# Performance work log

Measured on AMD Instinct MI355X. Metric: run time of the kernel, lower is better.

Reference implementation:

```python
import jax, jax.numpy as jnp
import numpy as np

OUT_CAPS_NUM = 16
OUT_CAPS_DIM = 512
ITER_NUM = 3
EPS = 1e-7


def setup_inputs() -> dict:
    key = jax.random.key(0)
    k_x, k_w = jax.random.split(key)
    x = jax.random.normal(k_x, (32, 128, 1024), dtype=jnp.float32)
    # xavier_normal-ish scale so tanh is not saturated
    W = jax.random.normal(k_w, (1024, OUT_CAPS_NUM * OUT_CAPS_DIM), dtype=jnp.float32) * 0.02
    return {"x": x, "W": W}


def _squash(S):
    # squash in source = divide by sqrt(||S||^2 + eps) (unit-ish norm)
    scale = jnp.sqrt(jnp.sum(S * S, axis=-1, keepdims=True) + EPS)
    return S / scale


def reference(x, W):
    b, s, _ = x.shape
    # caps_uhat: (b, s, out_caps_num, out_caps_dim)
    caps_uhat = jnp.tanh(jnp.einsum("bsd,dk->bsk", x, W)).reshape(
        b, s, OUT_CAPS_NUM, OUT_CAPS_DIM
    )
    B = jnp.zeros((b, s, OUT_CAPS_NUM), dtype=x.dtype)
    C_list = []
    B_logits = B
    V = None
    for _ in range(ITER_NUM):
        B_logits = B
        C = jax.nn.softmax(B, axis=2)          # (b, s, n)
        C_list.append(C)
        S = jnp.einsum("bsn,bsnd->bnd", C, caps_uhat)  # weighted sum over seq
        V = _squash(S)                          # (b, n, d)
        # agreement update: sum over caps dim
        B = jnp.einsum("bsnd,bnd->bsn", caps_uhat, V) + B
    C_ret = jnp.stack(C_list)                   # (iter, b, s, n)
    return (V, C_ret, B_logits)
```

## Files before the change

### kernel.cpp

```cpp
#include <hip/hip_runtime.h>
#include <math.h>

typedef float f32x4 __attribute__((ext_vector_type(4)));
typedef int   i32x4 __attribute__((ext_vector_type(4)));
typedef unsigned short u16;
typedef u16 u16x4 __attribute__((ext_vector_type(4)));

#define NG 8192
#define KG 1024

__device__ __forceinline__ u16 f2bf(float f) {
  unsigned u = __builtin_bit_cast(unsigned, f);
  u += 0x7fffu + ((u >> 16) & 1u);
  return (u16)(u >> 16);
}
__device__ __forceinline__ float bflo(unsigned u) {
  return __builtin_bit_cast(float, u << 16);
}
__device__ __forceinline__ float bfhi(unsigned u) {
  return __builtin_bit_cast(float, u & 0xffff0000u);
}

__device__ __forceinline__ void gload16(const void* g, void* l) {
  __builtin_amdgcn_global_load_lds(
      (const __attribute__((address_space(1))) void*)g,
      (__attribute__((address_space(3))) void*)l, 16, 0, 0);
}

__device__ __forceinline__ f32x4 mfma_bf16(i32x4 a, i32x4 b, f32x4 c) {
  asm("v_mfma_f32_16x16x32_bf16 %0, %1, %2, %0" : "+v"(c) : "v"(a), "v"(b));
  return c;
}

__device__ __forceinline__ float fast_tanh(float x) {
  float ax = fabsf(x);
  float e = __expf(-2.0f * ax);
  float r = (1.0f - e) * __frcp_rn(1.0f + e);
  return copysignf(r, x);
}

__global__ __launch_bounds__(256) void k_convx(const float* __restrict__ x,
                                               u16* __restrict__ xb) {
  int i = blockIdx.x * 256 + threadIdx.x;
  f32x4 v = ((const f32x4*)x)[i];
  u16x4 r = { f2bf(v.x), f2bf(v.y), f2bf(v.z), f2bf(v.w) };
  ((u16x4*)xb)[i] = r;
}

__global__ __launch_bounds__(256) void k_transW(const float* __restrict__ W,
                                                u16* __restrict__ wt) {
  __shared__ float tile[32][33];
  const int n0 = blockIdx.x * 32;
  const int k0 = blockIdx.y * 32;
  const int tx = threadIdx.x & 31;
  const int ty = threadIdx.x >> 5;
#pragma unroll
  for (int r = 0; r < 32; r += 8)
    tile[ty + r][tx] = W[(size_t)(k0 + ty + r) * NG + n0 + tx];
  __syncthreads();
#pragma unroll
  for (int r = 0; r < 32; r += 8)
    wt[(size_t)(n0 + ty + r) * KG + k0 + tx] = f2bf(tile[tx][ty + r]);
}

__global__ __launch_bounds__(256) void k_init(float* __restrict__ C0,
                                              float* __restrict__ Bws) {
  int i = blockIdx.x * 256 + threadIdx.x;
  f32x4 c = { 0.0625f, 0.0625f, 0.0625f, 0.0625f };
  f32x4 z = {};
  ((f32x4*)C0)[i] = c;
  ((f32x4*)Bws)[i] = z;
}

__global__ __launch_bounds__(256) void k_gemm_tanh(const u16* __restrict__ xb,
                                                   const u16* __restrict__ wt,
                                                   u16* __restrict__ uhat) {
  __shared__ u16 As[2][128 * 32];
  __shared__ u16 Bs[2][128 * 32];
  const int m0 = blockIdx.y * 128;
  const int n0 = blockIdx.x * 128;
  const int t = threadIdx.x;
  const int lane = t & 63;
  const int wave = t >> 6;
  const int wr = (wave >> 1) * 64;
  const int wc = (wave & 1) * 64;
  f32x4 acc[4][4] = {};

  const int r0 = t >> 2;
  const int r1 = 64 + (t >> 2);
  const int c0 = (t & 3) * 8;
  const u16* ga0 = xb + (size_t)(m0 + r0) * KG + c0;
  const u16* ga1 = xb + (size_t)(m0 + r1) * KG + c0;
  const u16* gb0 = wt + (size_t)(n0 + r0) * KG + c0;
  const u16* gb1 = wt + (size_t)(n0 + r1) * KG + c0;

  const int am = lane & 15;
  const int ak = (lane >> 4) * 8;

  for (int kt = 0; kt < KG; kt += 64) {
#pragma unroll
    for (int kh = 0; kh < 2; ++kh) {
      const int ko = kt + kh * 32;
      gload16(ga0 + ko, &As[kh][t * 8]);
      gload16(ga1 + ko, &As[kh][(256 + t) * 8]);
      gload16(gb0 + ko, &Bs[kh][t * 8]);
      gload16(gb1 + ko, &Bs[kh][(256 + t) * 8]);
    }
    __syncthreads();
#pragma unroll
    for (int kh = 0; kh < 2; ++kh) {
      i32x4 af[4], bf[4];
#pragma unroll
      for (int mi = 0; mi < 4; ++mi)
        af[mi] = *(const i32x4*)&As[kh][(wr + mi * 16 + am) * 32 + ak];
#pragma unroll
      for (int ni = 0; ni < 4; ++ni)
        bf[ni] = *(const i32x4*)&Bs[kh][(wc + ni * 16 + am) * 32 + ak];
#pragma unroll
      for (int mi = 0; mi < 4; ++mi)
#pragma unroll
        for (int ni = 0; ni < 4; ++ni)
          acc[mi][ni] = mfma_bf16(af[mi], bf[ni], acc[mi][ni]);
    }
    __syncthreads();
  }

  const int crow0 = (lane >> 4) * 4;
  const int ccol = lane & 15;
#pragma unroll
  for (int mi = 0; mi < 4; ++mi)
#pragma unroll
    for (int ni = 0; ni < 4; ++ni)
#pragma unroll
      for (int j = 0; j < 4; ++j) {
        int row = m0 + wr + mi * 16 + crow0 + j;
        int col = n0 + wc + ni * 16 + ccol;
        uhat[(size_t)row * NG + col] = f2bf(fast_tanh(acc[mi][ni][j]));
      }
}

template <int MODE>
__global__ __launch_bounds__(256) void k_fused(const u16* __restrict__ uhat,
                                               const float* __restrict__ C,
                                               float* __restrict__ dst) {
  __shared__ u16 Us[128 * 512];
  __shared__ float cl[128];
  __shared__ float Sred[4][512];
  const int n = blockIdx.x;
  const int b = blockIdx.y;
  const int t = threadIdx.x;
  const int lane = t & 63;
  const int wave = t >> 6;
  const u16* Ub = uhat + ((size_t)b * 128) * NG + n * 512;

  if (t < 128) cl[t] = C[((size_t)b * 128 + t) * 16 + n];

#pragma unroll 8
  for (int i = 0; i < 32; ++i) {
    const int row = i * 4 + wave;
    gload16(Ub + (size_t)row * NG + ((lane ^ (row & 7)) * 8),
            &Us[row * 512 + lane * 8]);
  }
  __syncthreads();

  float a[8] = {};
#pragma unroll 8
  for (int i = 0; i < 32; ++i) {
    const int s = wave + i * 4;
    i32x4 u = *(const i32x4*)&Us[s * 512 + ((lane ^ (s & 7)) * 8)];
    float c = cl[s];
    a[0] = fmaf(c, bflo(u.x), a[0]); a[1] = fmaf(c, bfhi(u.x), a[1]);
    a[2] = fmaf(c, bflo(u.y), a[2]); a[3] = fmaf(c, bfhi(u.y), a[3]);
    a[4] = fmaf(c, bflo(u.z), a[4]); a[5] = fmaf(c, bfhi(u.z), a[5]);
    a[6] = fmaf(c, bflo(u.w), a[6]); a[7] = fmaf(c, bfhi(u.w), a[7]);
  }
#pragma unroll
  for (int e = 0; e < 8; ++e) Sred[wave][lane * 8 + e] = a[e];
  __syncthreads();

  if (wave == 0) {
    float S[8];
    float ss = 0.f;
#pragma unroll
    for (int e = 0; e < 8; ++e) {
      int d = lane * 8 + e;
      S[e] = Sred[0][d] + Sred[1][d] + Sred[2][d] + Sred[3][d];
      ss = fmaf(S[e], S[e], ss);
    }
#pragma unroll
    for (int m = 1; m < 64; m <<= 1) ss += __shfl_xor(ss, m);
    float r = rsqrtf(ss + 1e-7f);
    if (MODE == 1) {
      float* vp = dst + ((size_t)b * 16 + n) * 512 + lane * 8;
      f32x4 v0 = { S[0] * r, S[1] * r, S[2] * r, S[3] * r };
      f32x4 v1 = { S[4] * r, S[5] * r, S[6] * r, S[7] * r };
      *(f32x4*)vp = v0;
      *(f32x4*)(vp + 4) = v1;
    } else {
#pragma unroll
      for (int e = 0; e < 8; ++e) Sred[0][lane * 8 + e] = S[e] * r;
    }
  }

  if (MODE == 0) {
    __syncthreads();
    const int s = t >> 1, h = t & 1;
    const float* Vl = &Sred[0][0];
    float dot = 0.f;
#pragma unroll 8
    for (int i = 0; i < 32; ++i) {
      const int chunk = h * 32 + i;
      i32x4 u = *(const i32x4*)&Us[s * 512 + ((chunk ^ (s & 7)) * 8)];
      const float* vp = Vl + chunk * 8;
      f32x4 v0 = *(const f32x4*)vp;
      f32x4 v1 = *(const f32x4*)(vp + 4);
      dot = fmaf(bflo(u.x), v0.x, dot);
      dot = fmaf(bfhi(u.x), v0.y, dot);
      dot = fmaf(bflo(u.y), v0.z, dot);
      dot = fmaf(bfhi(u.y), v0.w, dot);
      dot = fmaf(bflo(u.z), v1.x, dot);
      dot = fmaf(bfhi(u.z), v1.y, dot);
      dot = fmaf(bflo(u.w), v1.z, dot);
      dot = fmaf(bfhi(u.w), v1.w, dot);
    }
    dot += __shfl_xor(dot, 1);
    if (h == 0) dst[((size_t)b * 128 + s) * 16 + n] = dot;
  }
}

__global__ __launch_bounds__(256) void k_bsm(const float* __restrict__ dotB,
                                             float* __restrict__ Bws,
                                             float* __restrict__ Cnext,
                                             float* __restrict__ Blog) {
  int row = blockIdx.x * 256 + threadIdx.x;
  size_t o = (size_t)row * 16;
  f32x4 bv[4];
#pragma unroll
  for (int q = 0; q < 4; ++q) {
    f32x4 p = *(const f32x4*)(Bws + o + q * 4);
    f32x4 d = *(const f32x4*)(dotB + o + q * 4);
    bv[q].x = p.x + d.x; bv[q].y = p.y + d.y;
    bv[q].z = p.z + d.z; bv[q].w = p.w + d.w;
  }
  float mx = -1e30f;
#pragma unroll
  for (int q = 0; q < 4; ++q)
    mx = fmaxf(mx, fmaxf(fmaxf(bv[q].x, bv[q].y), fmaxf(bv[q].z, bv[q].w)));
  f32x4 ev[4];
  float sum = 0.f;
#pragma unroll
  for (int q = 0; q < 4; ++q) {
    ev[q].x = __expf(bv[q].x - mx); sum += ev[q].x;
    ev[q].y = __expf(bv[q].y - mx); sum += ev[q].y;
    ev[q].z = __expf(bv[q].z - mx); sum += ev[q].z;
    ev[q].w = __expf(bv[q].w - mx); sum += ev[q].w;
  }
  float r = __frcp_rn(sum);
#pragma unroll
  for (int q = 0; q < 4; ++q) {
    ev[q].x *= r; ev[q].y *= r; ev[q].z *= r; ev[q].w *= r;
    *(f32x4*)(Cnext + o + q * 4) = ev[q];
    *(f32x4*)(Bws + o + q * 4) = bv[q];
    if (Blog) *(f32x4*)(Blog + o + q * 4) = bv[q];
  }
}

extern "C" void kernel_launch(void* const* d_in, const int* in_sizes, int n_in,
                              void* d_out, int out_size, void* d_ws, size_t ws_size,
                              hipStream_t stream) {
  const float* x = (const float*)d_in[0];
  const float* W = (const float*)d_in[1];
  float* out = (float*)d_out;
  float* Vout = out;
  float* Cout = out + 262144;
  float* Blog = out + 262144 + 196608;

  char* ws = (char*)d_ws;
  u16* uhat = (u16*)ws;
  u16* xb   = (u16*)(ws + 67108864);
  u16* wt   = (u16*)(ws + 75497472);
  float* dotB = (float*)(ws + 92274688);
  float* Bws  = (float*)(ws + 92536832);

  k_convx<<<4096, 256, 0, stream>>>(x, xb);
  k_transW<<<dim3(256, 32), 256, 0, stream>>>(W, wt);
  k_init<<<64, 256, 0, stream>>>(Cout, Bws);
  k_gemm_tanh<<<dim3(64, 32), 256, 0, stream>>>(xb, wt, uhat);
  k_fused<0><<<dim3(16, 32), 256, 0, stream>>>(uhat, Cout, dotB);
  k_bsm<<<16, 256, 0, stream>>>(dotB, Bws, Cout + 65536, nullptr);
  k_fused<0><<<dim3(16, 32), 256, 0, stream>>>(uhat, Cout + 65536, dotB);
  k_bsm<<<16, 256, 0, stream>>>(dotB, Bws, Cout + 2 * 65536, Blog);
  k_fused<1><<<dim3(16, 32), 256, 0, stream>>>(uhat, Cout + 2 * 65536, Vout);
}
```

Baseline: 237.3 us.

## Split routing kernel over capsule-dim halves with deferred squash normalization

Each routing block now handles half of the 512-wide capsule dimension, doubling the grid from 512 to 1024 blocks and halving the LDS tile to 64KB. Partial squared norms and unnormalized partial dot products are written to workspace. The normalization is deferred: k_bsm combines the two halves and applies rsqrt, and a new k_vnorm kernel scales the final V. This aims to raise occupancy and CU utilization on a small grid, at the cost of an extra kernel launch and extra global traffic for partial results.

```diff
diff --git a/kernel.cpp b/kernel.cpp
--- a/kernel.cpp
+++ b/kernel.cpp
@@ -142,105 +142,109 @@
 template <int MODE>
 __global__ __launch_bounds__(256) void k_fused(const u16* __restrict__ uhat,
                                                const float* __restrict__ C,
-                                               float* __restrict__ dst) {
-  __shared__ u16 Us[128 * 512];
+                                               float* __restrict__ rdot,
+                                               float* __restrict__ ssp,
+                                               float* __restrict__ Vraw) {
+  __shared__ u16 Us[128 * 256];
+  __shared__ float Sred[8][256];
   __shared__ float cl[128];
-  __shared__ float Sred[4][512];
+  __shared__ float red[4];
   const int n = blockIdx.x;
   const int b = blockIdx.y;
+  const int H = blockIdx.z;
   const int t = threadIdx.x;
   const int lane = t & 63;
-  const int wave = t >> 6;
-  const u16* Ub = uhat + ((size_t)b * 128) * NG + n * 512;
+  const int w = t >> 6;
+  const int l32 = lane & 31;
+  const int hi = lane >> 5;
+  const u16* Ub = uhat + ((size_t)b * 128) * NG + n * 512 + H * 256;
 
   if (t < 128) cl[t] = C[((size_t)b * 128 + t) * 16 + n];
 
-#pragma unroll 8
-  for (int i = 0; i < 32; ++i) {
-    const int row = i * 4 + wave;
-    gload16(Ub + (size_t)row * NG + ((lane ^ (row & 7)) * 8),
-            &Us[row * 512 + lane * 8]);
+#pragma unroll
+  for (int i = 0; i < 16; ++i) {
+    const int r = w * 2 + i * 8;
+    const int rr = r + hi;
+    gload16(Ub + (size_t)rr * NG + ((l32 ^ (rr & 7)) * 8), &Us[r * 256]);
   }
   __syncthreads();
 
   float a[8] = {};
-#pragma unroll 8
-  for (int i = 0; i < 32; ++i) {
-    const int s = wave + i * 4;
-    i32x4 u = *(const i32x4*)&Us[s * 512 + ((lane ^ (s & 7)) * 8)];
-    float c = cl[s];
+#pragma unroll
+  for (int i = 0; i < 16; ++i) {
+    const int s = w * 2 + i * 8 + hi;
+    const float c = cl[s];
+    i32x4 u = *(const i32x4*)&Us[s * 256 + ((l32 ^ (s & 7)) * 8)];
     a[0] = fmaf(c, bflo(u.x), a[0]); a[1] = fmaf(c, bfhi(u.x), a[1]);
     a[2] = fmaf(c, bflo(u.y), a[2]); a[3] = fmaf(c, bfhi(u.y), a[3]);
     a[4] = fmaf(c, bflo(u.z), a[4]); a[5] = fmaf(c, bfhi(u.z), a[5]);
     a[6] = fmaf(c, bflo(u.w), a[6]); a[7] = fmaf(c, bfhi(u.w), a[7]);
   }
-#pragma unroll
-  for (int e = 0; e < 8; ++e) Sred[wave][lane * 8 + e] = a[e];
+  {
+    const int j = w * 2 + hi;
+#pragma unroll
+    for (int e = 0; e < 8; ++e) Sred[j][l32 * 8 + e] = a[e];
+  }
   __syncthreads();
 
-  if (wave == 0) {
-    float S[8];
-    float ss = 0.f;
-#pragma unroll
-    for (int e = 0; e < 8; ++e) {
-      int d = lane * 8 + e;
-      S[e] = Sred[0][d] + Sred[1][d] + Sred[2][d] + Sred[3][d];
-      ss = fmaf(S[e], S[e], ss);
-    }
-#pragma unroll
-    for (int m = 1; m < 64; m <<= 1) ss += __shfl_xor(ss, m);
-    float r = rsqrtf(ss + 1e-7f);
-    if (MODE == 1) {
-      float* vp = dst + ((size_t)b * 16 + n) * 512 + lane * 8;
-      f32x4 v0 = { S[0] * r, S[1] * r, S[2] * r, S[3] * r };
-      f32x4 v1 = { S[4] * r, S[5] * r, S[6] * r, S[7] * r };
-      *(f32x4*)vp = v0;
-      *(f32x4*)(vp + 4) = v1;
-    } else {
-#pragma unroll
-      for (int e = 0; e < 8; ++e) Sred[0][lane * 8 + e] = S[e] * r;
-    }
-  }
-
-  if (MODE == 0) {
-    __syncthreads();
-    const int s = t >> 1, h = t & 1;
-    const float* Vl = &Sred[0][0];
+  float S = 0.f;
+#pragma unroll
+  for (int j2 = 0; j2 < 8; ++j2) S += Sred[j2][t];
+  float ssq = S * S;
+#pragma unroll
+  for (int m = 1; m < 64; m <<= 1) ssq += __shfl_xor(ssq, m);
+  if (lane == 0) red[w] = ssq;
+  Sred[0][t] = S;
+  __syncthreads();
+  const float sstot = red[0] + red[1] + red[2] + red[3];
+  if (t == 0) ssp[H * 512 + b * 16 + n] = sstot;
+
+  if (MODE == 1) {
+    Vraw[((size_t)b * 16 + n) * 512 + H * 256 + t] = S;
+  } else {
+    const int s = t >> 1, u2 = t & 1;
     float dot = 0.f;
-#pragma unroll 8
-    for (int i = 0; i < 32; ++i) {
-      const int chunk = h * 32 + i;
-      i32x4 u = *(const i32x4*)&Us[s * 512 + ((chunk ^ (s & 7)) * 8)];
-      const float* vp = Vl + chunk * 8;
-      f32x4 v0 = *(const f32x4*)vp;
-      f32x4 v1 = *(const f32x4*)(vp + 4);
-      dot = fmaf(bflo(u.x), v0.x, dot);
-      dot = fmaf(bfhi(u.x), v0.y, dot);
-      dot = fmaf(bflo(u.y), v0.z, dot);
-      dot = fmaf(bfhi(u.y), v0.w, dot);
-      dot = fmaf(bflo(u.z), v1.x, dot);
-      dot = fmaf(bfhi(u.z), v1.y, dot);
-      dot = fmaf(bflo(u.w), v1.z, dot);
-      dot = fmaf(bfhi(u.w), v1.w, dot);
+#pragma unroll
+    for (int i = 0; i < 16; ++i) {
+      const int chunk = u2 * 16 + i;
+      i32x4 uv = *(const i32x4*)&Us[s * 256 + ((chunk ^ (s & 7)) * 8)];
+      f32x4 v0 = *(const f32x4*)&Sred[0][chunk * 8];
+      f32x4 v1 = *(const f32x4*)&Sred[0][chunk * 8 + 4];
+      dot = fmaf(bflo(uv.x), v0.x, dot);
+      dot = fmaf(bfhi(uv.x), v0.y, dot);
+      dot = fmaf(bflo(uv.y), v0.z, dot);
+      dot = fmaf(bfhi(uv.y), v0.w, dot);
+      dot = fmaf(bflo(uv.z), v1.x, dot);
+      dot = fmaf(bfhi(uv.z), v1.y, dot);
+      dot = fmaf(bflo(uv.w), v1.z, dot);
+      dot = fmaf(bfhi(uv.w), v1.w, dot);
     }
     dot += __shfl_xor(dot, 1);
-    if (h == 0) dst[((size_t)b * 128 + s) * 16 + n] = dot;
-  }
-}
-
-__global__ __launch_bounds__(256) void k_bsm(const float* __restrict__ dotB,
+    if (u2 == 0)
+      rdot[(size_t)H * 65536 + ((size_t)b * 128 + s) * 16 + n] = dot;
+  }
+}
+
+__global__ __launch_bounds__(256) void k_bsm(const float* __restrict__ rdot,
+                                             const float* __restrict__ ssp,
                                              float* __restrict__ Bws,
                                              float* __restrict__ Cnext,
                                              float* __restrict__ Blog) {
   int row = blockIdx.x * 256 + threadIdx.x;
+  int b = row >> 7;
   size_t o = (size_t)row * 16;
   f32x4 bv[4];
 #pragma unroll
   for (int q = 0; q < 4; ++q) {
-    f32x4 p = *(const f32x4*)(Bws + o + q * 4);
-    f32x4 d = *(const f32x4*)(dotB + o + q * 4);
-    bv[q].x = p.x + d.x; bv[q].y = p.y + d.y;
-    bv[q].z = p.z + d.z; bv[q].w = p.w + d.w;
+    f32x4 d0 = *(const f32x4*)(rdot + o + q * 4);
+    f32x4 d1 = *(const f32x4*)(rdot + 65536 + o + q * 4);
+    f32x4 s0 = *(const f32x4*)(ssp + b * 16 + q * 4);
+    f32x4 s1 = *(const f32x4*)(ssp + 512 + b * 16 + q * 4);
+    f32x4 p  = *(const f32x4*)(Bws + o + q * 4);
+    bv[q].x = p.x + (d0.x + d1.x) * rsqrtf(s0.x + s1.x + 1e-7f);
+    bv[q].y = p.y + (d0.y + d1.y) * rsqrtf(s0.y + s1.y + 1e-7f);
+    bv[q].z = p.z + (d0.z + d1.z) * rsqrtf(s0.z + s1.z + 1e-7f);
+    bv[q].w = p.w + (d0.w + d1.w) * rsqrtf(s0.w + s1.w + 1e-7f);
   }
   float mx = -1e30f;
 #pragma unroll
@@ -263,6 +267,19 @@
     *(f32x4*)(Bws + o + q * 4) = bv[q];
     if (Blog) *(f32x4*)(Blog + o + q * 4) = bv[q];
   }
+}
+
+__global__ __launch_bounds__(256) void k_vnorm(float* __restrict__ V,
+                                               const float* __restrict__ ssp) {
+  int i = blockIdx.x * 256 + threadIdx.x;
+  int bn = i >> 6;
+  float rs = rsqrtf(ssp[bn] + ssp[512 + bn] + 1e-7f);
+  f32x4 v0 = *(const f32x4*)(V + (size_t)i * 8);
+  f32x4 v1 = *(const f32x4*)(V + (size_t)i * 8 + 4);
+  v0.x *= rs; v0.y *= rs; v0.z *= rs; v0.w *= rs;
+  v1.x *= rs; v1.y *= rs; v1.z *= rs; v1.w *= rs;
+  *(f32x4*)(V + (size_t)i * 8) = v0;
+  *(f32x4*)(V + (size_t)i * 8 + 4) = v1;
 }
 
 extern "C" void kernel_launch(void* const* d_in, const int* in_sizes, int n_in,
@@ -276,19 +293,21 @@
   float* Blog = out + 262144 + 196608;
 
   char* ws = (char*)d_ws;
-  u16* uhat = (u16*)ws;
-  u16* xb   = (u16*)(ws + 67108864);
-  u16* wt   = (u16*)(ws + 75497472);
-  float* dotB = (float*)(ws + 92274688);
-  float* Bws  = (float*)(ws + 92536832);
+  u16* uhat  = (u16*)ws;
+  u16* xb    = (u16*)(ws + 67108864);
+  u16* wt    = (u16*)(ws + 75497472);
+  float* rdot = (float*)(ws + 92274688);
+  float* ssp  = (float*)(ws + 92798976);
+  float* Bws  = (float*)(ws + 92803072);
 
   k_convx<<<4096, 256, 0, stream>>>(x, xb);
   k_transW<<<dim3(256, 32), 256, 0, stream>>>(W, wt);
   k_init<<<64, 256, 0, stream>>>(Cout, Bws);
   k_gemm_tanh<<<dim3(64, 32), 256, 0, stream>>>(xb, wt, uhat);
-  k_fused<0><<<dim3(16, 32), 256, 0, stream>>>(uhat, Cout, dotB);
-  k_bsm<<<16, 256, 0, stream>>>(dotB, Bws, Cout + 65536, nullptr);
-  k_fused<0><<<dim3(16, 32), 256, 0, stream>>>(uhat, Cout + 65536, dotB);
-  k_bsm<<<16, 256, 0, stream>>>(dotB, Bws, Cout + 2 * 65536, Blog);
-  k_fused<1><<<dim3(16, 32), 256, 0, stream>>>(uhat, Cout + 2 * 65536, Vout);
-}
+  k_fused<0><<<dim3(16, 32, 2), 256, 0, stream>>>(uhat, Cout, rdot, ssp, nullptr);
+  k_bsm<<<16, 256, 0, stream>>>(rdot, ssp, Bws, Cout + 65536, nullptr);
+  k_fused<0><<<dim3(16, 32, 2), 256, 0, stream>>>(uhat, Cout + 65536, rdot, ssp, nullptr);
+  k_bsm<<<16, 256, 0, stream>>>(rdot, ssp, Bws, Cout + 2 * 65536, Blog);
+  k_fused<1><<<dim3(16, 32, 2), 256, 0, stream>>>(uhat, Cout + 2 * 65536, nullptr, ssp, Vout);
+  k_vnorm<<<128, 256, 0, stream>>>(Vout, ssp);
+}
```

Result: faster. 232.3 us (-2.1%).
